# Optimization experiments

Measured on AMD Instinct MI355X. Metric: run time of the kernel, lower is better.

The kernel has to match this reference:

```python
import jax, jax.numpy as jnp
import numpy as np

IN, OUT, BW = 2048, 2048, 8
L = 2 ** BW  # RNG sequence length
OFFSET = (2 * IN - 1) / 2.0  # module offset for non-scaled accumulation


def setup_inputs() -> dict:
    key = jax.random.key(0)
    ks = jax.random.split(key, 16)
    f = jnp.float32
    inp = {
        'input_r': jax.random.bernoulli(ks[0], 0.5, (1, IN)).astype(f),
        'input_i': jax.random.bernoulli(ks[1], 0.5, (1, IN)).astype(f),
        # SourceGen bipolar: round((w+1)/2 * 2^bw) in [0, 2^bw]
        'src_r': jax.random.randint(ks[2], (OUT, IN), 0, L + 1).astype(f),
        'src_i': jax.random.randint(ks[3], (OUT, IN), 0, L + 1).astype(f),
        # Sobol RNG of bitwidth 8 -> a permutation-like sequence of values 0..255
        'rng': jax.random.permutation(ks[4], L).astype(f),
    }
    names = ['idx1_fr_wr', 'idx0_fr_wr', 'idx1_fr_wi', 'idx0_fr_wi',
             'idx1_fi_wr', 'idx0_fi_wr', 'idx1_fi_wi', 'idx0_fi_wi']
    for i, n in enumerate(names):
        inp[n] = jax.random.randint(ks[5 + i], (OUT, IN), 0, L, dtype=jnp.int32)
    return inp


def _bit(src, rng, idx):
    # BSGen: bit = (source > rng[idx mod 2^bw])
    return (src > rng[idx % L]).astype(jnp.float32)


def _unary_kernel(x, src, rng, idx1, idx0):
    # kernel_1 weight = bit(src, idx1); kernel_0 weight = 1 - bit(src, idx0)
    w1 = _bit(src, rng, idx1)          # [O, I]
    w0 = 1.0 - _bit(src, rng, idx0)    # [O, I]
    # Linear(x) + Linear(1-x)  (no bias)
    return jnp.einsum('bi,oi->bo', x, w1) + jnp.einsum('bi,oi->bo', 1.0 - x, w0)


def reference(input_r, input_i, src_r, src_i, rng,
              idx1_fr_wr, idx0_fr_wr, idx1_fr_wi, idx0_fr_wi,
              idx1_fi_wr, idx0_fi_wr, idx1_fi_wi, idx0_fi_wi):
    o_fr_wr = _unary_kernel(input_r,       src_r, rng, idx1_fr_wr, idx0_fr_wr)
    o_fr_wi = _unary_kernel(input_r,       src_i, rng, idx1_fr_wi, idx0_fr_wi)
    o_fi_wr = _unary_kernel(input_i,       src_r, rng, idx1_fi_wr, idx0_fi_wr)
    o_fi_wi = _unary_kernel(1.0 - input_i, src_i, rng, idx1_fi_wi, idx0_fi_wi)
    # non-scaled accumulation (scaled=False), accumulators/out_accumulators start at 0
    acc_r = o_fr_wr + o_fi_wi - OFFSET
    out_r = (acc_r > 0.0).astype(jnp.float32)
    acc_i = o_fr_wi + o_fi_wr - OFFSET
    out_i = (acc_i > 0.0).astype(jnp.float32)
    return out_r, out_i
```

## Files before the change

kernel.cpp:

```cpp
#include <hip/hip_runtime.h>

#define IN_DIM 2048
#define OUT_DIM 2048
#define LVAL 256

__global__ __launch_bounds__(256) void ulc_kernel(
    const float* __restrict__ input_r, const float* __restrict__ input_i,
    const float* __restrict__ src_r,   const float* __restrict__ src_i,
    const float* __restrict__ rng,
    const int* __restrict__ i1_frwr, const int* __restrict__ i0_frwr,
    const int* __restrict__ i1_frwi, const int* __restrict__ i0_frwi,
    const int* __restrict__ i1_fiwr, const int* __restrict__ i0_fiwr,
    const int* __restrict__ i1_fiwi, const int* __restrict__ i0_fiwi,
    float* __restrict__ out)
{
    __shared__ float rng_s[LVAL];
    __shared__ int redA[4], redB[4];
    const int tid = threadIdx.x;
    if (tid < LVAL) rng_s[tid] = rng[tid];
    __syncthreads();

    const int o = blockIdx.x;
    const size_t rowoff = (size_t)o * IN_DIM;

    int accA = 0, accB = 0;

    #pragma unroll
    for (int j = 0; j < IN_DIM; j += 256 * 4) {
        const int c = j + tid * 4;
        const float4 sr4 = *(const float4*)(src_r + rowoff + c);
        const float4 si4 = *(const float4*)(src_i + rowoff + c);
        const float4 xr4 = *(const float4*)(input_r + c);
        const float4 xi4 = *(const float4*)(input_i + c);
        const int4 a1 = *(const int4*)(i1_frwr + rowoff + c);
        const int4 a0 = *(const int4*)(i0_frwr + rowoff + c);
        const int4 b1 = *(const int4*)(i1_frwi + rowoff + c);
        const int4 b0 = *(const int4*)(i0_frwi + rowoff + c);
        const int4 c1 = *(const int4*)(i1_fiwr + rowoff + c);
        const int4 c0 = *(const int4*)(i0_fiwr + rowoff + c);
        const int4 d1 = *(const int4*)(i1_fiwi + rowoff + c);
        const int4 d0 = *(const int4*)(i0_fiwi + rowoff + c);

        #define ELEM(e)                                                          \
        {                                                                        \
            const float sr = sr4.e, si = si4.e;                                  \
            const bool xr = xr4.e > 0.5f;                                        \
            const bool xi = xi4.e > 0.5f;                                        \
            const int frwr = xr  ? (sr > rng_s[a1.e & 255]) : !(sr > rng_s[a0.e & 255]); \
            const int frwi = xr  ? (si > rng_s[b1.e & 255]) : !(si > rng_s[b0.e & 255]); \
            const int fiwr = xi  ? (sr > rng_s[c1.e & 255]) : !(sr > rng_s[c0.e & 255]); \
            const int fiwi = !xi ? (si > rng_s[d1.e & 255]) : !(si > rng_s[d0.e & 255]); \
            accA += frwr + fiwi;                                                 \
            accB += frwi + fiwr;                                                 \
        }
        ELEM(x) ELEM(y) ELEM(z) ELEM(w)
        #undef ELEM
    }

    #pragma unroll
    for (int off = 32; off > 0; off >>= 1) {
        accA += __shfl_down(accA, off);
        accB += __shfl_down(accB, off);
    }
    const int wid = tid >> 6;
    if ((tid & 63) == 0) { redA[wid] = accA; redB[wid] = accB; }
    __syncthreads();
    if (tid == 0) {
        const int sA = redA[0] + redA[1] + redA[2] + redA[3];
        const int sB = redB[0] + redB[1] + redB[2] + redB[3];
        out[o]           = (sA >= 2048) ? 1.0f : 0.0f;
        out[OUT_DIM + o] = (sB >= 2048) ? 1.0f : 0.0f;
    }
}

extern "C" void kernel_launch(void* const* d_in, const int* in_sizes, int n_in,
                              void* d_out, int out_size, void* d_ws, size_t ws_size,
                              hipStream_t stream) {
    const float* input_r = (const float*)d_in[0];
    const float* input_i = (const float*)d_in[1];
    const float* src_r   = (const float*)d_in[2];
    const float* src_i   = (const float*)d_in[3];
    const float* rng     = (const float*)d_in[4];
    const int* i1_frwr = (const int*)d_in[5];
    const int* i0_frwr = (const int*)d_in[6];
    const int* i1_frwi = (const int*)d_in[7];
    const int* i0_frwi = (const int*)d_in[8];
    const int* i1_fiwr = (const int*)d_in[9];
    const int* i0_fiwr = (const int*)d_in[10];
    const int* i1_fiwi = (const int*)d_in[11];
    const int* i0_fiwi = (const int*)d_in[12];
    float* out = (float*)d_out;

    ulc_kernel<<<dim3(OUT_DIM), dim3(256), 0, stream>>>(
        input_r, input_i, src_r, src_i, rng,
        i1_frwr, i0_frwr, i1_frwi, i0_frwi,
        i1_fiwr, i0_fiwr, i1_fiwi, i0_fiwi,
        out);
}
```

Before: 31.90 us.

## Stream row tiles into LDS via async global_load_lds with double buffering

```diff
diff --git a/kernel.cpp b/kernel.cpp
--- a/kernel.cpp
+++ b/kernel.cpp
@@ -2,7 +2,11 @@
 
 #define IN_DIM 2048
 #define OUT_DIM 2048
-#define LVAL 256
+#define TILE 512
+#define NT 4
+
+typedef const __attribute__((address_space(1))) unsigned int* gp_t;
+typedef __attribute__((address_space(3))) unsigned int* lp_t;
 
 __global__ __launch_bounds__(256) void ulc_kernel(
     const float* __restrict__ input_r, const float* __restrict__ input_i,
@@ -14,47 +18,81 @@
     const int* __restrict__ i1_fiwi, const int* __restrict__ i0_fiwi,
     float* __restrict__ out)
 {
-    __shared__ float rng_s[LVAL];
+    __shared__ unsigned int tile[2][10 * TILE];
+    __shared__ float rng_s[256];
     __shared__ int redA[4], redB[4];
-    const int tid = threadIdx.x;
-    if (tid < LVAL) rng_s[tid] = rng[tid];
-    __syncthreads();
 
-    const int o = blockIdx.x;
-    const size_t rowoff = (size_t)o * IN_DIM;
+    const int tid  = threadIdx.x;
+    const int wid  = tid >> 6;
+    const int lane = tid & 63;
+    const int o    = blockIdx.x;
+    const size_t row = (size_t)o * IN_DIM;
+
+    rng_s[tid] = rng[tid];
+
+    float2 xr2[NT], xi2[NT];
+    #pragma unroll
+    for (int t = 0; t < NT; ++t) {
+        xr2[t] = *(const float2*)(input_r + t * TILE + tid * 2);
+        xi2[t] = *(const float2*)(input_i + t * TILE + tid * 2);
+    }
+    bool xrb[2 * NT], xib[2 * NT];
+    #pragma unroll
+    for (int t = 0; t < NT; ++t) {
+        xrb[2*t] = xr2[t].x > 0.5f;  xrb[2*t+1] = xr2[t].y > 0.5f;
+        xib[2*t] = xi2[t].x > 0.5f;  xib[2*t+1] = xi2[t].y > 0.5f;
+    }
+    __builtin_amdgcn_sched_barrier(0);
+
+    #define SEG(s, P, t, b)                                                         \
+        __builtin_amdgcn_global_load_lds(                                           \
+            (gp_t)((const unsigned int*)(P) + row + (size_t)(t) * TILE              \
+                   + ((s) & 1) * 256 + lane * 4),                                   \
+            (lp_t)(&tile[(b)][(s) * 256]), 16, 0, 0);
+
+    #define STAGE(t, b)                                                                          \
+        if (wid == 0)      { SEG(0,src_r,t,b)   SEG(1,src_r,t,b)   SEG(2,src_i,t,b)              \
+                             SEG(3,src_i,t,b)   SEG(4,i1_frwr,t,b) }                             \
+        else if (wid == 1) { SEG(5,i1_frwr,t,b) SEG(6,i0_frwr,t,b) SEG(7,i0_frwr,t,b)            \
+                             SEG(8,i1_frwi,t,b) SEG(9,i1_frwi,t,b) }                             \
+        else if (wid == 2) { SEG(10,i0_frwi,t,b) SEG(11,i0_frwi,t,b) SEG(12,i1_fiwr,t,b)         \
+                             SEG(13,i1_fiwr,t,b) SEG(14,i0_fiwr,t,b) }                           \
+        else               { SEG(15,i0_fiwr,t,b) SEG(16,i1_fiwi,t,b) SEG(17,i1_fiwi,t,b)         \
+                             SEG(18,i0_fiwi,t,b) SEG(19,i0_fiwi,t,b) }
 
     int accA = 0, accB = 0;
 
+    STAGE(0, 0)
+
     #pragma unroll
-    for (int j = 0; j < IN_DIM; j += 256 * 4) {
-        const int c = j + tid * 4;
-        const float4 sr4 = *(const float4*)(src_r + rowoff + c);
-        const float4 si4 = *(const float4*)(src_i + rowoff + c);
-        const float4 xr4 = *(const float4*)(input_r + c);
-        const float4 xi4 = *(const float4*)(input_i + c);
-        const int4 a1 = *(const int4*)(i1_frwr + rowoff + c);
-        const int4 a0 = *(const int4*)(i0_frwr + rowoff + c);
-        const int4 b1 = *(const int4*)(i1_frwi + rowoff + c);
-        const int4 b0 = *(const int4*)(i0_frwi + rowoff + c);
-        const int4 c1 = *(const int4*)(i1_fiwr + rowoff + c);
-        const int4 c0 = *(const int4*)(i0_fiwr + rowoff + c);
-        const int4 d1 = *(const int4*)(i1_fiwi + rowoff + c);
-        const int4 d0 = *(const int4*)(i0_fiwi + rowoff + c);
+    for (int t = 0; t < NT; ++t) {
+        if (t + 1 < NT) { STAGE(t + 1, (t + 1) & 1) }
+        if (t + 1 < NT) asm volatile("s_waitcnt vmcnt(5) lgkmcnt(0)" ::: "memory");
+        else            asm volatile("s_waitcnt vmcnt(0) lgkmcnt(0)" ::: "memory");
+        __builtin_amdgcn_s_barrier();
+        __builtin_amdgcn_sched_barrier(0);
 
-        #define ELEM(e)                                                          \
-        {                                                                        \
-            const float sr = sr4.e, si = si4.e;                                  \
-            const bool xr = xr4.e > 0.5f;                                        \
-            const bool xi = xi4.e > 0.5f;                                        \
-            const int frwr = xr  ? (sr > rng_s[a1.e & 255]) : !(sr > rng_s[a0.e & 255]); \
-            const int frwi = xr  ? (si > rng_s[b1.e & 255]) : !(si > rng_s[b0.e & 255]); \
-            const int fiwr = xi  ? (sr > rng_s[c1.e & 255]) : !(sr > rng_s[c0.e & 255]); \
-            const int fiwi = !xi ? (si > rng_s[d1.e & 255]) : !(si > rng_s[d0.e & 255]); \
-            accA += frwr + fiwi;                                                 \
-            accB += frwi + fiwr;                                                 \
+        const unsigned int* tl = &tile[t & 1][0];
+        const int j0 = tid * 2;
+        #pragma unroll
+        for (int q = 0; q < 2; ++q) {
+            const int j = j0 + q;
+            const bool xr = xrb[2*t + q], xi = xib[2*t + q];
+            const float sr = __uint_as_float(tl[0 * TILE + j]);
+            const float si = __uint_as_float(tl[1 * TILE + j]);
+            const int ia = tl[(xr ? 2 : 3) * TILE + j] & 255;
+            const int ib = tl[(xr ? 4 : 5) * TILE + j] & 255;
+            const int ic = tl[(xi ? 6 : 7) * TILE + j] & 255;
+            const int id = tl[(xi ? 9 : 8) * TILE + j] & 255;
+            const bool cA = sr > rng_s[ia];
+            const bool cB = si > rng_s[ib];
+            const bool cC = sr > rng_s[ic];
+            const bool cD = si > rng_s[id];
+            accA += (int)(cA == xr) + (int)(cD != xi);
+            accB += (int)(cB == xr) + (int)(cC == xi);
         }
-        ELEM(x) ELEM(y) ELEM(z) ELEM(w)
-        #undef ELEM
+        __builtin_amdgcn_sched_barrier(0);
+        __builtin_amdgcn_s_barrier();
     }
 
     #pragma unroll
@@ -62,7 +100,6 @@
         accA += __shfl_down(accA, off);
         accB += __shfl_down(accB, off);
     }
-    const int wid = tid >> 6;
     if ((tid & 63) == 0) { redA[wid] = accA; redB[wid] = accB; }
     __syncthreads();
     if (tid == 0) {
```

Result: faster. 30.97 us (-2.9%).

## Issue all row loads upfront via inline asm with staged vmcnt waits

Applied to the files above, without the earlier changes.

```diff
diff --git a/kernel.cpp b/kernel.cpp
--- a/kernel.cpp
+++ b/kernel.cpp
@@ -2,9 +2,16 @@
 
 #define IN_DIM 2048
 #define OUT_DIM 2048
-#define LVAL 256
 
-__global__ __launch_bounds__(256) void ulc_kernel(
+typedef __attribute__((ext_vector_type(4))) int int4v;
+
+#define GLOAD(dst, ptr, voff)                                   \
+    asm volatile("global_load_dwordx4 %0, %1, %2"               \
+                 : "=v"(dst)                                    \
+                 : "v"(voff), "s"(ptr)                          \
+                 : "memory")
+
+__global__ __launch_bounds__(256, 4) void ulc_kernel(
     const float* __restrict__ input_r, const float* __restrict__ input_i,
     const float* __restrict__ src_r,   const float* __restrict__ src_i,
     const float* __restrict__ rng,
@@ -14,48 +21,69 @@
     const int* __restrict__ i1_fiwi, const int* __restrict__ i0_fiwi,
     float* __restrict__ out)
 {
-    __shared__ float rng_s[LVAL];
+    __shared__ float rng_s[256];
     __shared__ int redA[4], redB[4];
     const int tid = threadIdx.x;
-    if (tid < LVAL) rng_s[tid] = rng[tid];
+    rng_s[tid] = rng[tid];
+
+    const int o = blockIdx.x;
+
+    const float4 xrA = *(const float4*)(input_r + tid * 4);
+    const float4 xiA = *(const float4*)(input_i + tid * 4);
+    const float4 xrB = *(const float4*)(input_r + 1024 + tid * 4);
+    const float4 xiB = *(const float4*)(input_i + 1024 + tid * 4);
+
     __syncthreads();
 
-    const int o = blockIdx.x;
-    const size_t rowoff = (size_t)o * IN_DIM;
+    const bool xr[8] = { xrA.x > 0.5f, xrA.y > 0.5f, xrA.z > 0.5f, xrA.w > 0.5f,
+                         xrB.x > 0.5f, xrB.y > 0.5f, xrB.z > 0.5f, xrB.w > 0.5f };
+    const bool xi[8] = { xiA.x > 0.5f, xiA.y > 0.5f, xiA.z > 0.5f, xiA.w > 0.5f,
+                         xiB.x > 0.5f, xiB.y > 0.5f, xiB.z > 0.5f, xiB.w > 0.5f };
+
+    const unsigned v0 = (unsigned)o * 8192u + (unsigned)tid * 16u;
+    const unsigned v1 = v0 + 4096u;
+
+    int4v sr0, si0, a1_0, a0_0, b1_0, b0_0, c1_0, c0_0, d1_0, d0_0;
+    int4v sr1, si1, a1_1, a0_1, b1_1, b0_1, c1_1, c0_1, d1_1, d0_1;
+
+    GLOAD(sr0, src_r,   v0);  GLOAD(si0, src_i,   v0);
+    GLOAD(a1_0, i1_frwr, v0); GLOAD(a0_0, i0_frwr, v0);
+    GLOAD(b1_0, i1_frwi, v0); GLOAD(b0_0, i0_frwi, v0);
+    GLOAD(c1_0, i1_fiwr, v0); GLOAD(c0_0, i0_fiwr, v0);
+    GLOAD(d1_0, i1_fiwi, v0); GLOAD(d0_0, i0_fiwi, v0);
+    GLOAD(sr1, src_r,   v1);  GLOAD(si1, src_i,   v1);
+    GLOAD(a1_1, i1_frwr, v1); GLOAD(a0_1, i0_frwr, v1);
+    GLOAD(b1_1, i1_frwi, v1); GLOAD(b0_1, i0_frwi, v1);
+    GLOAD(c1_1, i1_fiwr, v1); GLOAD(c0_1, i0_fiwr, v1);
+    GLOAD(d1_1, i1_fiwi, v1); GLOAD(d0_1, i0_fiwi, v1);
 
     int accA = 0, accB = 0;
 
-    #pragma unroll
-    for (int j = 0; j < IN_DIM; j += 256 * 4) {
-        const int c = j + tid * 4;
-        const float4 sr4 = *(const float4*)(src_r + rowoff + c);
-        const float4 si4 = *(const float4*)(src_i + rowoff + c);
-        const float4 xr4 = *(const float4*)(input_r + c);
-        const float4 xi4 = *(const float4*)(input_i + c);
-        const int4 a1 = *(const int4*)(i1_frwr + rowoff + c);
-        const int4 a0 = *(const int4*)(i0_frwr + rowoff + c);
-        const int4 b1 = *(const int4*)(i1_frwi + rowoff + c);
-        const int4 b0 = *(const int4*)(i0_frwi + rowoff + c);
-        const int4 c1 = *(const int4*)(i1_fiwr + rowoff + c);
-        const int4 c0 = *(const int4*)(i0_fiwr + rowoff + c);
-        const int4 d1 = *(const int4*)(i1_fiwi + rowoff + c);
-        const int4 d0 = *(const int4*)(i0_fiwi + rowoff + c);
+    #define ELEM(k, q, xq)                                                   \
+    {                                                                        \
+        const float sr = __int_as_float(sr##k[q]);                           \
+        const float si = __int_as_float(si##k[q]);                           \
+        const bool xr_ = xr[xq], xi_ = xi[xq];                               \
+        const int ia = (xr_ ? a1_##k[q] : a0_##k[q]) & 255;                  \
+        const int ib = (xr_ ? b1_##k[q] : b0_##k[q]) & 255;                  \
+        const int ic = (xi_ ? c1_##k[q] : c0_##k[q]) & 255;                  \
+        const int id = (xi_ ? d0_##k[q] : d1_##k[q]) & 255;                  \
+        const bool cA = sr > rng_s[ia];                                      \
+        const bool cB = si > rng_s[ib];                                      \
+        const bool cC = sr > rng_s[ic];                                      \
+        const bool cD = si > rng_s[id];                                      \
+        accA += (int)(cA == xr_) + (int)(cD != xi_);                         \
+        accB += (int)(cB == xr_) + (int)(cC == xi_);                         \
+    }
 
-        #define ELEM(e)                                                          \
-        {                                                                        \
-            const float sr = sr4.e, si = si4.e;                                  \
-            const bool xr = xr4.e > 0.5f;                                        \
-            const bool xi = xi4.e > 0.5f;                                        \
-            const int frwr = xr  ? (sr > rng_s[a1.e & 255]) : !(sr > rng_s[a0.e & 255]); \
-            const int frwi = xr  ? (si > rng_s[b1.e & 255]) : !(si > rng_s[b0.e & 255]); \
-            const int fiwr = xi  ? (sr > rng_s[c1.e & 255]) : !(sr > rng_s[c0.e & 255]); \
-            const int fiwi = !xi ? (si > rng_s[d1.e & 255]) : !(si > rng_s[d0.e & 255]); \
-            accA += frwr + fiwi;                                                 \
-            accB += frwi + fiwr;                                                 \
-        }
-        ELEM(x) ELEM(y) ELEM(z) ELEM(w)
-        #undef ELEM
-    }
+    asm volatile("s_waitcnt vmcnt(10)" ::: "memory");
+    __builtin_amdgcn_sched_barrier(0);
+    ELEM(0, 0, 0) ELEM(0, 1, 1) ELEM(0, 2, 2) ELEM(0, 3, 3)
+
+    asm volatile("s_waitcnt vmcnt(0)" ::: "memory");
+    __builtin_amdgcn_sched_barrier(0);
+    ELEM(1, 0, 4) ELEM(1, 1, 5) ELEM(1, 2, 6) ELEM(1, 3, 7)
+    #undef ELEM
 
     #pragma unroll
     for (int off = 32; off > 0; off >>= 1) {
```

After: 30.32 us. 1.05x faster.
